# Kernel tuning notes

Hardware: AMD Instinct MI355X
Metric: run time of the kernel (lower is better)

The kernel has to match this reference:

```python
import jax, jax.numpy as jnp
import numpy as np
import math

HIDDEN = 1024
HEADS = 8
HEAD = HIDDEN // HEADS
B, S = 2, 2048
SCALE_BASE = 512
EPS = 1e-5


def _xpos(x, downscale=False):
    # x: [..., S, d]  (canonical RetNet XPOS: rotate_every_two + xpos scaling)
    d = x.shape[-1]
    s = x.shape[-2]
    half = d // 2
    scale_vec = (jnp.arange(0, d, 2, dtype=jnp.float32) + 0.4 * d) / (1.4 * d)  # [half]
    pos = jnp.arange(s, dtype=jnp.float32)
    scale = scale_vec[None, :] ** (pos[:, None] / SCALE_BASE)                    # [S, half]
    inv_freq = 1.0 / (10000.0 ** (jnp.arange(half, dtype=jnp.float32) / half))
    ang = pos[:, None] * inv_freq[None, :]                                       # [S, half]
    sin, cos = jnp.sin(ang), jnp.cos(ang)
    if downscale:
        scale = 1.0 / scale
    sinp = jnp.repeat(sin * scale, 2, axis=-1)  # duplicate_interleave -> [S, d]
    cosp = jnp.repeat(cos * scale, 2, axis=-1)
    x1, x2 = x[..., ::2], x[..., 1::2]
    rot = jnp.stack([-x2, x1], axis=-1).reshape(x.shape)  # rotate_every_two
    return x * cosp + rot * sinp


def _gammas(h):
    return 1.0 - jnp.exp(jnp.linspace(math.log(1.0 / 32), math.log(1.0 / 512), h)).astype(jnp.float32)


def setup_inputs() -> dict:
    key = jax.random.key(0)
    ks = jax.random.split(key, 6)
    X = jax.random.normal(ks[0], (B, S, HIDDEN), dtype=jnp.float32)
    W_Q = jax.random.normal(ks[1], (HEADS, HIDDEN, HEAD), dtype=jnp.float32) / HIDDEN
    W_K = jax.random.normal(ks[2], (HEADS, HIDDEN, HEAD), dtype=jnp.float32) / HIDDEN
    W_V = jax.random.normal(ks[3], (HEADS, HIDDEN, HEAD), dtype=jnp.float32) / HIDDEN
    W_G = jax.random.normal(ks[4], (HIDDEN, HIDDEN), dtype=jnp.float32) / HIDDEN
    W_O = jax.random.normal(ks[5], (HIDDEN, HIDDEN), dtype=jnp.float32) / HIDDEN
    gn_weight = jnp.ones((HIDDEN,), dtype=jnp.float32)
    gn_bias = jnp.zeros((HIDDEN,), dtype=jnp.float32)
    return dict(X=X, W_Q=W_Q, W_K=W_K, W_V=W_V, W_G=W_G, W_O=W_O,
                gn_weight=gn_weight, gn_bias=gn_bias)


def reference(X, W_Q, W_K, W_V, W_G, W_O, gn_weight, gn_bias):
    b, s, _ = X.shape
    h, _, dv = W_V.shape
    Q = _xpos(jnp.einsum('bse,hed->bhsd', X, W_Q))
    K = _xpos(jnp.einsum('bse,hed->bhsd', X, W_K), downscale=True)
    V = jnp.einsum('bse,hed->bhsd', X, W_V)
    gam = _gammas(h)
    n = jnp.arange(s)
    diff = n[:, None] - n[None, :]
    mask = diff >= 0
    # per-head causal decay mask D[h, n, m] = gamma_h**(n-m) for n>=m else 0
    D = jnp.where(mask[None],
                  gam[:, None, None] ** jnp.where(mask, diff, 0)[None].astype(jnp.float32),
                  0.0)                                             # [H,S,S]
    scores = jnp.einsum('bhsd,bhtd->bhst', Q, K) * D[None]         # [B,H,S,S]
    Y = jnp.einsum('bhst,bhtv->bhsv', scores, V)                   # [B,H,S,dv]
    Y = jnp.transpose(Y, (0, 2, 1, 3))                             # [B,S,H,dv] (head concat)
    # GroupNorm(heads, v_dim) over flattened (B*S, v_dim): normalize within each head group
    mu = Y.mean(-1, keepdims=True)
    var = Y.var(-1, keepdims=True)
    Yn = ((Y - mu) / jnp.sqrt(var + EPS)).reshape(b, s, h * dv) * gn_weight + gn_bias
    gate = X @ W_G
    gate = gate * jax.nn.sigmoid(gate)  # swish
    return (gate * Yn) @ W_O
```

## Files before the change

kernel.cpp:

```cpp
#include <hip/hip_runtime.h>
#include <hip/hip_bf16.h>
#include <math.h>

namespace {

constexpr int Bc = 2;
constexpr int Sc = 2048;
constexpr int Ec = 1024;
constexpr int Hc = 8;
constexpr int Dc = 128;
constexpr int Mc = Bc * Sc;

typedef unsigned short u16;
typedef u16    u16x8  __attribute__((ext_vector_type(8)));
typedef u16    u16x4  __attribute__((ext_vector_type(4)));
typedef __bf16 bf16x8 __attribute__((ext_vector_type(8)));
typedef float  f32x4  __attribute__((ext_vector_type(4)));

static __device__ inline bf16x8 asbf(u16x8 v) { return __builtin_bit_cast(bf16x8, v); }

static __device__ inline f32x4 mfma16(u16x8 a, u16x8 b, f32x4 c) {
    return __builtin_amdgcn_mfma_f32_16x16x32_bf16(asbf(a), asbf(b), c, 0, 0, 0);
}

static __device__ inline u16 f2bf(float f) {
    unsigned u = __builtin_bit_cast(unsigned, f);
    return (u16)((u + 0x7fffu + ((u >> 16) & 1u)) >> 16);
}
static __device__ inline float bf2f(u16 h) {
    unsigned u = ((unsigned)h) << 16;
    return __builtin_bit_cast(float, u);
}

static __device__ inline void gload16(const u16* g, u16* l) {
    __builtin_amdgcn_global_load_lds(
        (__attribute__((address_space(1))) void*)const_cast<u16*>(g),
        (__attribute__((address_space(3))) void*)l,
        16, 0, 0);
}

__global__ __launch_bounds__(256) void convX(const float* __restrict__ in,
                                             u16* __restrict__ out, int n8)
{
    int i = blockIdx.x * 256 + threadIdx.x;
    if (i >= n8) return;
    float4 a = *(const float4*)(in + (size_t)i * 8);
    float4 b = *(const float4*)(in + (size_t)i * 8 + 4);
    u16x8 o;
    o[0] = f2bf(a.x); o[1] = f2bf(a.y); o[2] = f2bf(a.z); o[3] = f2bf(a.w);
    o[4] = f2bf(b.x); o[5] = f2bf(b.y); o[6] = f2bf(b.z); o[7] = f2bf(b.w);
    *(u16x8*)(out + (size_t)i * 8) = o;
}

__global__ __launch_bounds__(256) void tconvH(const float* __restrict__ p0,
                                              const float* __restrict__ p1,
                                              const float* __restrict__ p2,
                                              u16* __restrict__ out)
{
    const int z = blockIdx.z;
    const float* ip = (z < 8 ? p0 : z < 16 ? p1 : p2) + (size_t)(z & 7) * Ec * Dc;
    u16* op = out + (size_t)z * Dc * Ec;
    __shared__ float tile[32][33];
    const int r0 = blockIdx.x * 32, c0 = blockIdx.y * 32;
    const int ty = threadIdx.x >> 5, tx = threadIdx.x & 31;
#pragma unroll
    for (int i = ty; i < 32; i += 8) tile[i][tx] = ip[(size_t)(r0 + i) * Dc + c0 + tx];
    __syncthreads();
#pragma unroll
    for (int i = ty; i < 32; i += 8) op[(size_t)(c0 + i) * Ec + r0 + tx] = f2bf(tile[tx][i]);
}

__global__ __launch_bounds__(256) void tconvSq(const float* __restrict__ p0,
                                               const float* __restrict__ p1,
                                               u16* __restrict__ out)
{
    const int z = blockIdx.z;
    const float* ip = z == 0 ? p0 : p1;
    u16* op = out + (size_t)z * Ec * Ec;
    __shared__ float tile[32][33];
    const int r0 = blockIdx.x * 32, c0 = blockIdx.y * 32;
    const int ty = threadIdx.x >> 5, tx = threadIdx.x & 31;
#pragma unroll
    for (int i = ty; i < 32; i += 8) tile[i][tx] = ip[(size_t)(r0 + i) * Ec + c0 + tx];
    __syncthreads();
#pragma unroll
    for (int i = ty; i < 32; i += 8) op[(size_t)(c0 + i) * Ec + r0 + tx] = f2bf(tile[tx][i]);
}

__global__ __launch_bounds__(256) void trigk(float2* __restrict__ tabQ,
                                             float2* __restrict__ tabK)
{
    int t = blockIdx.x * 256 + threadIdx.x;
    int s = t >> 6, ip = t & 63;
    float sv = (2.f * (float)ip + 51.2f) * (1.f / 179.2f);
    float sc = exp2f(((float)s * (1.f / 512.f)) * log2f(sv));
    float freq = exp2f(-(float)ip * (13.287712379549449f / 64.f));
    float ang = (float)s * freq;
    float sn, cs;
    sincosf(ang, &sn, &cs);
    tabQ[t] = make_float2(cs * sc, sn * sc);
    tabK[t] = make_float2(cs / sc, sn / sc);
}

#define GCORE_STAGE(lA, lB, k0)                                   \
    do {                                                          \
        gload16(Ag + (k0),                  (lA) + w * 1024);     \
        gload16(Ag + 16 * Ec + (k0),        (lA) + w * 1024 + 512);\
        gload16(Bg + (k0),                  (lB) + w * 1024);     \
        gload16(Bg + 16 * Ec + (k0),        (lB) + w * 1024 + 512);\
    } while (0)

#define GCORE_COMPUTE(lA, lB)                                                 \
    do {                                                                      \
        u16x8 bfr[8];                                                         \
        _Pragma("unroll")                                                     \
        for (int ct = 0; ct < 8; ++ct)                                        \
            bfr[ct] = *(const u16x8*)&(lB)[(ct * 16 + rl) * 32 + hi * 8];     \
        _Pragma("unroll")                                                     \
        for (int rt = 0; rt < 2; ++rt) {                                      \
            u16x8 afr = *(const u16x8*)&(lA)[(w * 32 + rt * 16 + rl) * 32 + hi * 8]; \
            _Pragma("unroll")                                                 \
            for (int ct = 0; ct < 8; ++ct)                                    \
                acc[rt][ct] = mfma16(bfr[ct], afr, acc[rt][ct]);              \
        }                                                                     \
    } while (0)

#define GCORE_SYNC()                                              \
    do {                                                          \
        asm volatile("s_waitcnt vmcnt(0)" ::: "memory");          \
        __builtin_amdgcn_s_barrier();                             \
    } while (0)

__global__ __launch_bounds__(256) void mgemm4(const u16* __restrict__ A,
                                              const u16* __restrict__ Ball,
                                              u16* __restrict__ Qo,
                                              u16* __restrict__ Ko,
                                              u16* __restrict__ Vo,
                                              u16* __restrict__ Go,
                                              const float2* __restrict__ tabQ,
                                              const float2* __restrict__ tabK)
{
    const int t = threadIdx.x;
    const int lane = t & 63, w = t >> 6;
    const int rl = lane & 15, hi = lane >> 4;
    const int r0 = blockIdx.x * 128;
    const int wsel = blockIdx.y >> 3;
    const int n0 = (blockIdx.y & 7) * 128;
    const u16* Bt = Ball + (size_t)wsel * Ec * Ec;

    __shared__ u16 As0[4096], As1[4096], Bs0[4096], Bs1[4096];

    f32x4 acc[2][8] = {};

    const u16* Ag = A  + (size_t)(r0 + w * 32 + (lane >> 2)) * Ec + (lane & 3) * 8;
    const u16* Bg = Bt + (size_t)(n0 + w * 32 + (lane >> 2)) * Ec + (lane & 3) * 8;

    GCORE_STAGE(As0, Bs0, 0);
    GCORE_SYNC();
    for (int k0 = 0; k0 < Ec; k0 += 64) {
        GCORE_STAGE(As1, Bs1, k0 + 32);
        GCORE_COMPUTE(As0, Bs0);
        GCORE_SYNC();
        if (k0 + 64 < Ec) GCORE_STAGE(As0, Bs0, k0 + 64);
        GCORE_COMPUTE(As1, Bs1);
        GCORE_SYNC();
    }

    u16* Cout = wsel == 0 ? Qo : wsel == 1 ? Ko : wsel == 2 ? Vo : Go;
    const float2* tab = wsel == 0 ? tabQ : tabK;

#pragma unroll
    for (int rt = 0; rt < 2; ++rt) {
        const int row = r0 + w * 32 + rt * 16 + rl;
#pragma unroll
        for (int ct = 0; ct < 8; ++ct) {
            const int col0 = n0 + ct * 16 + hi * 4;
            f32x4 v = acc[rt][ct];
            if (wsel <= 1) {
                const size_t tb = (size_t)(row & 2047) * 64 + ((col0 >> 1) & 63);
                const float2 c0 = tab[tb];
                const float2 c1 = tab[tb + 1];
                float e0 = v[0], o0 = v[1], e1 = v[2], o1 = v[3];
                v[0] = e0 * c0.x - o0 * c0.y;
                v[1] = o0 * c0.x + e0 * c0.y;
                v[2] = e1 * c1.x - o1 * c1.y;
                v[3] = o1 * c1.x + e1 * c1.y;
            } else if (wsel == 3) {
#pragma unroll
                for (int r = 0; r < 4; ++r) v[r] = v[r] / (1.f + expf(-v[r]));
            }
            u16x4 pk;
#pragma unroll
            for (int r = 0; r < 4; ++r) pk[r] = f2bf(v[r]);
            *(u16x4*)(Cout + (size_t)row * Ec + col0) = pk;
        }
    }
}

__global__ __launch_bounds__(256) void mgemmO(const u16* __restrict__ A,
                                              const u16* __restrict__ Bt,
                                              float* __restrict__ Cout)
{
    const int t = threadIdx.x;
    const int lane = t & 63, w = t >> 6;
    const int rl = lane & 15, hi = lane >> 4;
    const int r0 = blockIdx.x * 128;
    const int n0 = blockIdx.y * 128;

    __shared__ u16 As0[4096], As1[4096], Bs0[4096], Bs1[4096];

    f32x4 acc[2][8] = {};

    const u16* Ag = A  + (size_t)(r0 + w * 32 + (lane >> 2)) * Ec + (lane & 3) * 8;
    const u16* Bg = Bt + (size_t)(n0 + w * 32 + (lane >> 2)) * Ec + (lane & 3) * 8;

    GCORE_STAGE(As0, Bs0, 0);
    GCORE_SYNC();
    for (int k0 = 0; k0 < Ec; k0 += 64) {
        GCORE_STAGE(As1, Bs1, k0 + 32);
        GCORE_COMPUTE(As0, Bs0);
        GCORE_SYNC();
        if (k0 + 64 < Ec) GCORE_STAGE(As0, Bs0, k0 + 64);
        GCORE_COMPUTE(As1, Bs1);
        GCORE_SYNC();
    }

#pragma unroll
    for (int rt = 0; rt < 2; ++rt) {
        const int row = r0 + w * 32 + rt * 16 + rl;
#pragma unroll
        for (int ct = 0; ct < 8; ++ct) {
            const int col0 = n0 + ct * 16 + hi * 4;
            *(f32x4*)(Cout + (size_t)row * Ec + col0) = acc[rt][ct];
        }
    }
}

__global__ __launch_bounds__(256) void ret_gn(const u16* __restrict__ Q,
                                              const u16* __restrict__ K,
                                              const u16* __restrict__ V,
                                              const u16* __restrict__ G,
                                              const float* __restrict__ gw,
                                              const float* __restrict__ gbias,
                                              u16* __restrict__ Z)
{
    const int t = threadIdx.x, lane = t & 63, w = t >> 6;
    const int rl = lane & 15, hi = lane >> 4;
    const int id = blockIdx.x;
    const int bh = id & 15;
    const int a  = id >> 4;
    const int rb = (a < 16) ? (31 - a) : (a - 16);
    const int b = bh >> 3, h = bh & 7;

    __shared__ u16 Ks[2][64][136];
    __shared__ u16 Vt[2][128][68];
    __shared__ u16 Ss[64][72];

    const float lga = -3.4657359027997265f;
    const float lgb = -6.2383246250395075f;
    const float gamma = 1.f - expf(lga + (float)h * (lgb - lga) * (1.f / 7.f));
    const float lg2 = log2f(gamma);

    int c_lo = 0;
    {
        float cut = 9.2103404f / (-logf(gamma));
        int mmin = rb * 64 - (int)cut;
        if (mmin > 0) c_lo = mmin >> 6;
    }

    const int ki = t >> 2,        kq = (t & 3) * 32;
    const int vm4 = (t & 15) * 4, vd = (t >> 4) * 8;
    const u16* Kg0 = K + (size_t)(b * Sc) * Ec + h * Dc;
    const u16* Vg0 = V + (size_t)(b * Sc) * Ec + h * Dc;

    u16x8 kreg[4], vreg[4];
    {
        const u16* Kg = Kg0 + (size_t)(c_lo * 64 + ki) * Ec + kq;
#pragma unroll
        for (int r = 0; r < 4; ++r) kreg[r] = *(const u16x8*)(Kg + r * 8);
        const u16* Vg = Vg0 + (size_t)(c_lo * 64 + vm4) * Ec + vd;
#pragma unroll
        for (int r = 0; r < 4; ++r) vreg[r] = *(const u16x8*)(Vg + (size_t)r * Ec);
    }

    {
        const int i = t >> 2, q = (t & 3) * 32;
        const u16* Qg = Q + (size_t)(b * Sc + rb * 64 + i) * Ec + h * Dc + q;
        u16x8 v0 = *(const u16x8*)(Qg);
        u16x8 v1 = *(const u16x8*)(Qg + 8);
        u16x8 v2 = *(const u16x8*)(Qg + 16);
        u16x8 v3 = *(const u16x8*)(Qg + 24);
        *(u16x8*)&Ks[0][i][q]      = v0;
        *(u16x8*)&Ks[0][i][q + 8]  = v1;
        *(u16x8*)&Ks[0][i][q + 16] = v2;
        *(u16x8*)&Ks[0][i][q + 24] = v3;
    }
    __syncthreads();
    u16x8 qf[4][4];
#pragma unroll
    for (int nt = 0; nt < 4; ++nt)
#pragma unroll
        for (int ks = 0; ks < 4; ++ks)
            qf[nt][ks] = *(const u16x8*)&Ks[0][nt * 16 + rl][ks * 32 + hi * 8];
    __syncthreads();

    float mf[4];
#pragma unroll
    for (int reg = 0; reg < 4; ++reg)
        mf[reg] = exp2f(-lg2 * (float)(w * 16 + hi * 4 + reg));
    float nf[4];
#pragma unroll
    for (int nt = 0; nt < 4; ++nt)
        nf[nt] = exp2f(lg2 * (float)((rb - c_lo) * 64 + nt * 16 + rl));
    const float ginv64 = exp2f(-lg2 * 64.f);

    f32x4 yacc[8] = {};

    for (int c = c_lo; c <= rb; ++c) {
        const int cur = c & 1;
#pragma unroll
        for (int r = 0; r < 4; ++r)
            *(u16x8*)&Ks[cur][ki][kq + r * 8] = kreg[r];
#pragma unroll
        for (int j = 0; j < 8; ++j) {
            u16x4 p;
            p[0] = vreg[0][j]; p[1] = vreg[1][j]; p[2] = vreg[2][j]; p[3] = vreg[3][j];
            *(u16x4*)&Vt[cur][vd + j][vm4] = p;
        }
        __syncthreads();
        if (c < rb) {
            const u16* Kg = Kg0 + (size_t)((c + 1) * 64 + ki) * Ec + kq;
#pragma unroll
            for (int r = 0; r < 4; ++r) kreg[r] = *(const u16x8*)(Kg + r * 8);
            const u16* Vg = Vg0 + (size_t)((c + 1) * 64 + vm4) * Ec + vd;
#pragma unroll
            for (int r = 0; r < 4; ++r) vreg[r] = *(const u16x8*)(Vg + (size_t)r * Ec);
        }

        __builtin_amdgcn_s_setprio(1);
        u16x8 kf[4];
#pragma unroll
        for (int ks = 0; ks < 4; ++ks)
            kf[ks] = *(const u16x8*)&Ks[cur][w * 16 + rl][ks * 32 + hi * 8];
#pragma unroll
        for (int nt = 0; nt < 4; ++nt) {
            f32x4 s = {};
#pragma unroll
            for (int ks = 0; ks < 4; ++ks)
                s = mfma16(kf[ks], qf[nt][ks], s);
            u16x4 pk;
#pragma unroll
            for (int reg = 0; reg < 4; ++reg) {
                float wgt = nf[nt] * mf[reg];
                if (c == rb && (w * 16 + hi * 4 + reg) > (nt * 16 + rl)) wgt = 0.f;
                pk[reg] = f2bf(s[reg] * wgt);
            }
            *(u16x4*)&Ss[nt * 16 + rl][w * 16 + hi * 4] = pk;
        }
        __builtin_amdgcn_s_setprio(0);
        __syncthreads();

        u16x8 sf0 = *(const u16x8*)&Ss[w * 16 + rl][hi * 8];
        u16x8 sf1 = *(const u16x8*)&Ss[w * 16 + rl][32 + hi * 8];
        __builtin_amdgcn_s_setprio(1);
#pragma unroll
        for (int ct = 0; ct < 8; ++ct) {
            u16x8 vf0 = *(const u16x8*)&Vt[cur][ct * 16 + rl][hi * 8];
            u16x8 vf1 = *(const u16x8*)&Vt[cur][ct * 16 + rl][32 + hi * 8];
            yacc[ct] = mfma16(vf0, sf0, yacc[ct]);
            yacc[ct] = mfma16(vf1, sf1, yacc[ct]);
        }
        __builtin_amdgcn_s_setprio(0);
#pragma unroll
        for (int nt = 0; nt < 4; ++nt) nf[nt] *= ginv64;
    }

    const int nloc = w * 16 + rl;
    const size_t row = (size_t)(b * Sc + rb * 64 + nloc);
    float s = 0.f, sq = 0.f;
#pragma unroll
    for (int ct = 0; ct < 8; ++ct)
#pragma unroll
        for (int reg = 0; reg < 4; ++reg) {
            float v = yacc[ct][reg];
            s += v; sq += v * v;
        }
    s  += __shfl_xor(s, 16);  sq += __shfl_xor(sq, 16);
    s  += __shfl_xor(s, 32);  sq += __shfl_xor(sq, 32);
    const float mu  = s * (1.f / 128.f);
    const float var = sq * (1.f / 128.f) - mu * mu;
    const float inv = rsqrtf(var + 1e-5f);
#pragma unroll
    for (int ct = 0; ct < 8; ++ct) {
        const int col0 = h * Dc + ct * 16 + hi * 4;
        const f32x4 w4 = *(const f32x4*)(gw + col0);
        const f32x4 b4 = *(const f32x4*)(gbias + col0);
        const u16x4 g4 = *(const u16x4*)(G + row * Ec + col0);
        u16x4 z4;
#pragma unroll
        for (int reg = 0; reg < 4; ++reg)
            z4[reg] = f2bf(((yacc[ct][reg] - mu) * inv * w4[reg] + b4[reg]) * bf2f(g4[reg]));
        *(u16x4*)(Z + row * Ec + col0) = z4;
    }
}

}

extern "C" void kernel_launch(void* const* d_in, const int* in_sizes, int n_in,
                              void* d_out, int out_size, void* d_ws, size_t ws_size,
                              hipStream_t stream)
{
    const float* X    = (const float*)d_in[0];
    const float* W_Q  = (const float*)d_in[1];
    const float* W_K  = (const float*)d_in[2];
    const float* W_V  = (const float*)d_in[3];
    const float* W_G  = (const float*)d_in[4];
    const float* W_O  = (const float*)d_in[5];
    const float* gw   = (const float*)d_in[6];
    const float* gb   = (const float*)d_in[7];

    char* ws = (char*)d_ws;
    const size_t NX = (size_t)Mc * Ec;
    u16*    Xb   = (u16*)ws;                ws += NX * 2;
    u16*    WqT  = (u16*)ws;                ws += (size_t)Ec * Ec * 2;
    u16*    WkT  = (u16*)ws;                ws += (size_t)Ec * Ec * 2;
    u16*    WvT  = (u16*)ws;                ws += (size_t)Ec * Ec * 2;
    u16*    WgT  = (u16*)ws;                ws += (size_t)Ec * Ec * 2;
    u16*    WoT  = (u16*)ws;                ws += (size_t)Ec * Ec * 2;
    float2* tabQ = (float2*)ws;             ws += (size_t)Sc * 64 * sizeof(float2);
    float2* tabK = (float2*)ws;             ws += (size_t)Sc * 64 * sizeof(float2);
    u16*    Qb   = (u16*)ws;                ws += NX * 2;
    u16*    Kb   = (u16*)ws;                ws += NX * 2;
    u16*    Vb   = (u16*)ws;                ws += NX * 2;
    u16*    Gb   = (u16*)ws;                ws += NX * 2;
    u16*    Zb   = (u16*)ws;                ws += NX * 2;
    (void)WkT; (void)WvT; (void)WgT;

    dim3 blk(256);
    convX<<<dim3((int)(NX / 8 / 256)), blk, 0, stream>>>(X, Xb, (int)(NX / 8));
    tconvH<<<dim3(32, 4, 24), blk, 0, stream>>>(W_Q, W_K, W_V, WqT);
    tconvSq<<<dim3(32, 32, 2), blk, 0, stream>>>(W_G, W_O, WgT);
    trigk<<<dim3(Sc * 64 / 256), blk, 0, stream>>>(tabQ, tabK);

    mgemm4<<<dim3(Mc / 128, 32), blk, 0, stream>>>(Xb, WqT, Qb, Kb, Vb, Gb, tabQ, tabK);

    ret_gn<<<dim3(512), blk, 0, stream>>>(Qb, Kb, Vb, Gb, gw, gb, Zb);

    mgemmO<<<dim3(Mc / 128, Ec / 128), blk, 0, stream>>>(Zb, WoT, (float*)d_out);
}
```

Measured before the change: 151.4 us.

## Rewrite fused QKVG projection GEMM with 256x256 tiles, 8 waves, swizzled LDS

Replaces the 128x128, 4-wave projection GEMM with a 256x256 tile per 512-thread block, each wave computing a 128x64 sub-tile. K-tiles grow to 64, the LDS layout uses an XOR swizzle to avoid bank conflicts, and the double buffer is pipelined with a partial vmcnt wait so the next tile's loads overlap compute. It also raises MFMA wave priority. This aims to increase operand reuse per LDS byte and reduce global traffic per FLOP. In exchange it uses more registers (32 accumulators per lane), 128 KB of LDS, and launches fewer blocks (256), which may hurt occupancy and tail balance.

```diff
diff --git a/kernel.cpp b/kernel.cpp
--- a/kernel.cpp
+++ b/kernel.cpp
@@ -100,6 +100,121 @@
     sincosf(ang, &sn, &cs);
     tabQ[t] = make_float2(cs * sc, sn * sc);
     tabK[t] = make_float2(cs / sc, sn / sc);
+}
+
+__global__ __launch_bounds__(512, 2) void mgemm4(const u16* __restrict__ A,
+                                                 const u16* __restrict__ Ball,
+                                                 u16* __restrict__ Qo,
+                                                 u16* __restrict__ Ko,
+                                                 u16* __restrict__ Vo,
+                                                 u16* __restrict__ Go,
+                                                 const float2* __restrict__ tabQ,
+                                                 const float2* __restrict__ tabK)
+{
+    const int t = threadIdx.x, lane = t & 63, wid = t >> 6;
+    const int wm = wid >> 2, wn = wid & 3;
+    const int rl = lane & 15, hi = lane >> 4;
+    const int r0 = blockIdx.x * 256;
+    const int wsel = blockIdx.y >> 2;
+    const int n0 = (blockIdx.y & 3) * 256;
+    const u16* Bt = Ball + (size_t)wsel * Ec * Ec;
+
+    __shared__ u16 lds[2][2][256 * 64];
+
+    f32x4 acc[8][4] = {};
+
+    const int srow = lane >> 3;
+    const int scol = (((lane & 7) ^ srow) << 3);
+    const u16* Asrc = A  + (size_t)(r0 + wid * 32 + srow) * Ec + scol;
+    const u16* Bsrc = Bt + (size_t)(n0 + wid * 32 + srow) * Ec + scol;
+
+#define STAGE256(tile, buf)                                                     \
+    do {                                                                        \
+        const int _k0 = (tile) * 64;                                            \
+        _Pragma("unroll")                                                       \
+        for (int i = 0; i < 4; ++i) {                                           \
+            gload16(Asrc + (size_t)(i * 8) * Ec + _k0,                          \
+                    &lds[buf][0][(wid * 32 + i * 8) * 64]);                     \
+            gload16(Bsrc + (size_t)(i * 8) * Ec + _k0,                          \
+                    &lds[buf][1][(wid * 32 + i * 8) * 64]);                     \
+        }                                                                       \
+    } while (0)
+
+    STAGE256(0, 0);
+    for (int tt = 0; tt < 16; ++tt) {
+        const int buf = tt & 1;
+        if (tt + 1 < 16) {
+            STAGE256(tt + 1, buf ^ 1);
+            asm volatile("s_waitcnt vmcnt(8)" ::: "memory");
+        } else {
+            asm volatile("s_waitcnt vmcnt(0)" ::: "memory");
+        }
+        __builtin_amdgcn_s_barrier();
+
+        u16x8 breg[4][2];
+#pragma unroll
+        for (int cf = 0; cf < 4; ++cf)
+#pragma unroll
+            for (int ks = 0; ks < 2; ++ks) {
+                const int row = wn * 64 + cf * 16 + rl;
+                breg[cf][ks] = *(const u16x8*)
+                    &lds[buf][1][row * 64 + ((ks * 32 + hi * 8) ^ ((rl & 7) << 3))];
+            }
+#pragma unroll
+        for (int q = 0; q < 4; ++q) {
+            u16x8 areg[2][2];
+#pragma unroll
+            for (int rfi = 0; rfi < 2; ++rfi)
+#pragma unroll
+                for (int ks = 0; ks < 2; ++ks) {
+                    const int row = wm * 128 + (q * 2 + rfi) * 16 + rl;
+                    areg[rfi][ks] = *(const u16x8*)
+                        &lds[buf][0][row * 64 + ((ks * 32 + hi * 8) ^ ((rl & 7) << 3))];
+                }
+            __builtin_amdgcn_s_setprio(1);
+#pragma unroll
+            for (int rfi = 0; rfi < 2; ++rfi)
+#pragma unroll
+                for (int cf = 0; cf < 4; ++cf)
+#pragma unroll
+                    for (int ks = 0; ks < 2; ++ks)
+                        acc[q * 2 + rfi][cf] =
+                            mfma16(breg[cf][ks], areg[rfi][ks], acc[q * 2 + rfi][cf]);
+            __builtin_amdgcn_s_setprio(0);
+        }
+        __builtin_amdgcn_s_barrier();
+    }
+#undef STAGE256
+
+    u16* Cout = wsel == 0 ? Qo : wsel == 1 ? Ko : wsel == 2 ? Vo : Go;
+    const float2* tab = wsel == 0 ? tabQ : tabK;
+
+#pragma unroll
+    for (int rf = 0; rf < 8; ++rf) {
+        const int row = r0 + wm * 128 + rf * 16 + rl;
+#pragma unroll
+        for (int cf = 0; cf < 4; ++cf) {
+            const int col0 = n0 + wn * 64 + cf * 16 + hi * 4;
+            f32x4 v = acc[rf][cf];
+            if (wsel <= 1) {
+                const size_t tb = (size_t)(row & 2047) * 64 + ((col0 >> 1) & 63);
+                const float2 c0 = tab[tb];
+                const float2 c1 = tab[tb + 1];
+                float e0 = v[0], o0 = v[1], e1 = v[2], o1 = v[3];
+                v[0] = e0 * c0.x - o0 * c0.y;
+                v[1] = o0 * c0.x + e0 * c0.y;
+                v[2] = e1 * c1.x - o1 * c1.y;
+                v[3] = o1 * c1.x + e1 * c1.y;
+            } else if (wsel == 3) {
+#pragma unroll
+                for (int r = 0; r < 4; ++r) v[r] = v[r] / (1.f + expf(-v[r]));
+            }
+            u16x4 pk;
+#pragma unroll
+            for (int r = 0; r < 4; ++r) pk[r] = f2bf(v[r]);
+            *(u16x4*)(Cout + (size_t)row * Ec + col0) = pk;
+        }
+    }
 }
 
 #define GCORE_STAGE(lA, lB, k0)                                   \
@@ -130,72 +245,6 @@
         asm volatile("s_waitcnt vmcnt(0)" ::: "memory");          \
         __builtin_amdgcn_s_barrier();                             \
     } while (0)
-
-__global__ __launch_bounds__(256) void mgemm4(const u16* __restrict__ A,
-                                              const u16* __restrict__ Ball,
-                                              u16* __restrict__ Qo,
-                                              u16* __restrict__ Ko,
-                                              u16* __restrict__ Vo,
-                                              u16* __restrict__ Go,
-                                              const float2* __restrict__ tabQ,
-                                              const float2* __restrict__ tabK)
-{
-    const int t = threadIdx.x;
-    const int lane = t & 63, w = t >> 6;
-    const int rl = lane & 15, hi = lane >> 4;
-    const int r0 = blockIdx.x * 128;
-    const int wsel = blockIdx.y >> 3;
-    const int n0 = (blockIdx.y & 7) * 128;
-    const u16* Bt = Ball + (size_t)wsel * Ec * Ec;
-
-    __shared__ u16 As0[4096], As1[4096], Bs0[4096], Bs1[4096];
-
-    f32x4 acc[2][8] = {};
-
-    const u16* Ag = A  + (size_t)(r0 + w * 32 + (lane >> 2)) * Ec + (lane & 3) * 8;
-    const u16* Bg = Bt + (size_t)(n0 + w * 32 + (lane >> 2)) * Ec + (lane & 3) * 8;
-
-    GCORE_STAGE(As0, Bs0, 0);
-    GCORE_SYNC();
-    for (int k0 = 0; k0 < Ec; k0 += 64) {
-        GCORE_STAGE(As1, Bs1, k0 + 32);
-        GCORE_COMPUTE(As0, Bs0);
-        GCORE_SYNC();
-        if (k0 + 64 < Ec) GCORE_STAGE(As0, Bs0, k0 + 64);
-        GCORE_COMPUTE(As1, Bs1);
-        GCORE_SYNC();
-    }
-
-    u16* Cout = wsel == 0 ? Qo : wsel == 1 ? Ko : wsel == 2 ? Vo : Go;
-    const float2* tab = wsel == 0 ? tabQ : tabK;
-
-#pragma unroll
-    for (int rt = 0; rt < 2; ++rt) {
-        const int row = r0 + w * 32 + rt * 16 + rl;
-#pragma unroll
-        for (int ct = 0; ct < 8; ++ct) {
-            const int col0 = n0 + ct * 16 + hi * 4;
-            f32x4 v = acc[rt][ct];
-            if (wsel <= 1) {
-                const size_t tb = (size_t)(row & 2047) * 64 + ((col0 >> 1) & 63);
-                const float2 c0 = tab[tb];
-                const float2 c1 = tab[tb + 1];
-                float e0 = v[0], o0 = v[1], e1 = v[2], o1 = v[3];
-                v[0] = e0 * c0.x - o0 * c0.y;
-                v[1] = o0 * c0.x + e0 * c0.y;
-                v[2] = e1 * c1.x - o1 * c1.y;
-                v[3] = o1 * c1.x + e1 * c1.y;
-            } else if (wsel == 3) {
-#pragma unroll
-                for (int r = 0; r < 4; ++r) v[r] = v[r] / (1.f + expf(-v[r]));
-            }
-            u16x4 pk;
-#pragma unroll
-            for (int r = 0; r < 4; ++r) pk[r] = f2bf(v[r]);
-            *(u16x4*)(Cout + (size_t)row * Ec + col0) = pk;
-        }
-    }
-}
 
 __global__ __launch_bounds__(256) void mgemmO(const u16* __restrict__ A,
                                               const u16* __restrict__ Bt,
@@ -442,7 +491,7 @@
     tconvSq<<<dim3(32, 32, 2), blk, 0, stream>>>(W_G, W_O, WgT);
     trigk<<<dim3(Sc * 64 / 256), blk, 0, stream>>>(tabQ, tabK);
 
-    mgemm4<<<dim3(Mc / 128, 32), blk, 0, stream>>>(Xb, WqT, Qb, Kb, Vb, Gb, tabQ, tabK);
+    mgemm4<<<dim3(Mc / 256, 16), dim3(512), 0, stream>>>(Xb, WqT, Qb, Kb, Vb, Gb, tabQ, tabK);
 
     ret_gn<<<dim3(512), blk, 0, stream>>>(Qb, Kb, Vb, Gb, gw, gb, Zb);
 
```

Result: faster. 133.6 us (-11.8%).
